# Performance work log

Hardware: AMD Instinct MI355X
Metric: run time of the kernel (lower is better)

## Reference

```python
import jax, jax.numpy as jnp
import numpy as np

BITS = 4
QMAX = (1 << BITS) - 1      # 15
QHALF = 1 << (BITS - 1)     # 8
B, S = 4, 2048
IN, OUT, FP = 4096, 4096, 256
INT = IN - FP


def setup_inputs() -> dict:
    key = jax.random.key(0)
    k0, k1, k2, k3 = jax.random.split(key, 4)
    x = jax.random.normal(k0, (B, S, IN), dtype=jnp.float16)
    # disjoint outlier / int feature index sets (QUIK splits columns by outlier-ness)
    perm = np.random.default_rng(0).permutation(IN)
    fp_indices = jnp.sort(jnp.asarray(perm[:FP], dtype=jnp.int32))
    int_indices = jnp.sort(jnp.asarray(perm[FP:], dtype=jnp.int32))
    # unpacked int4 weight values in [-8, 7] (torch stores these packed 2-per-uint8)
    int_weight = jax.random.randint(k1, (OUT, INT), -QHALF, QHALF, dtype=jnp.int8)
    weights_scales = (jax.random.uniform(k2, (OUT, 1), dtype=jnp.float32) * 0.01 + 1e-3).astype(jnp.float16)
    fp_weight = (jax.random.normal(k3, (OUT, FP), dtype=jnp.float32) * 0.02).astype(jnp.float16)
    bias = jnp.zeros((OUT,), dtype=jnp.float16)
    # reduced_w[j] = w_scale[j] * sum_k int_weight[j, k]  (precomputed zero-point correction)
    reduced_w = (weights_scales.astype(jnp.float32)[:, 0] * jnp.sum(int_weight.astype(jnp.float32), axis=1)).reshape(1, OUT).astype(jnp.float16)
    return {"x": x, "int_weight": int_weight, "fp_weight": fp_weight, "bias": bias,
            "weights_scales": weights_scales, "reduced_w": reduced_w,
            "int_indices": int_indices, "fp_indices": fp_indices}


def reference(x, int_weight, fp_weight, bias, weights_scales, reduced_w, int_indices, fp_indices):
    b, s, in_feat = x.shape
    xf = x.reshape(-1, in_feat)                       # [N, in] tokens
    int_x = xf[:, int_indices].astype(jnp.float32)    # [N, INT]
    fp_x = xf[:, fp_indices].astype(jnp.float32)      # [N, FP] outliers stay fp16-precision
    # asymmetric per-token quantization (quik.asymmetric.quantize)
    mn = jnp.min(int_x, axis=1, keepdims=True)
    mx = jnp.max(int_x, axis=1, keepdims=True)
    scale = jnp.maximum((mx - mn) / QMAX, 1e-8)       # [N,1]
    q = (jnp.clip(jnp.round((int_x - mn) / scale), 0, QMAX) - QHALF).astype(jnp.int8)  # signed int4 in [-8,7]
    zero = scale * QHALF + mn                         # [N,1] shifted zero point
    # int4 GEMM (quik.matmul.int4Matmul), int32 accumulate
    int_res = jnp.einsum('nk,ok->no', q, int_weight, preferred_element_type=jnp.int32)
    # fp outlier branch fused with bias (F.linear)
    fp_res = fp_x @ fp_weight.astype(jnp.float32).T + bias.astype(jnp.float32)[None, :]
    # quik.asymmetric.dequantize: q*scale_x*scale_w + zero_x*reduced_w + fp_result
    out = (int_res.astype(jnp.float32) * scale * weights_scales.astype(jnp.float32)[:, 0][None, :]
           + zero * reduced_w.astype(jnp.float32) + fp_res)
    return out.astype(jnp.float16).reshape(b, s, -1)
```

## Files before the change

### kernel.cpp

```cpp
#include <hip/hip_runtime.h>
#include <hip/hip_bf16.h>
#include <stdint.h>

#define N_TOK 8192
#define IN_F  4096
#define OUT_F 4096
#define FP_F  256
#define INT_F 3840
#define PROW  1920

typedef int    v4i   __attribute__((ext_vector_type(4)));
typedef int    v16i  __attribute__((ext_vector_type(16)));
typedef float  v16f  __attribute__((ext_vector_type(16)));
typedef __bf16 bf16x8 __attribute__((ext_vector_type(8)));

#define WS_QP   0u
#define WS_WP   15728640u
#define WS_FPX  23592960u
#define WS_WFP  27787264u
#define WS_F1   29884416u
#define WS_F2   29917184u
#define WS_F3   29949952u
#define WS_NEED 29982720u


__global__ __launch_bounds__(256) void zero_out_kernel(uint4* __restrict__ o) {
  o[(size_t)blockIdx.x * 256 + threadIdx.x] = uint4{0, 0, 0, 0};
}

__global__ __launch_bounds__(256) void prep_kernel(
    const float* __restrict__ x,
    const int* __restrict__ int_idx, const int* __restrict__ fp_idx,
    const int* __restrict__ int_w, const float* __restrict__ fp_w,
    uint8_t* __restrict__ qp, uint8_t* __restrict__ wp,
    __hip_bfloat16* __restrict__ fpx, __hip_bfloat16* __restrict__ wfp,
    float* __restrict__ f1, float* __restrict__ f2, float* __restrict__ f3) {
  __shared__ uint2 qb[240];
  __shared__ float smn[4], smx[4], ssum[4];
  __shared__ float s_mn, s_inv, s_sc;

  int tid = threadIdx.x;
  int blk = blockIdx.x;

  if (blk >= N_TOK) {
    int pb = blk - N_TOK;
    if (pb < OUT_F * 480 / 256) {
      int t = pb * 256 + tid;
      int r = t / 480, u = t % 480;
      int g = u >> 1, h = u & 1;
      const int* src = int_w + (size_t)r * INT_F + g * 16 + h * 4;
      int4 lo = *(const int4*)src;
      int4 hi = *(const int4*)(src + 8);
      uint32_t o = (uint32_t)((lo.x + 8) & 15) | (uint32_t)((hi.x + 8) & 15) << 4 |
                   (uint32_t)((lo.y + 8) & 15) << 8 | (uint32_t)((hi.y + 8) & 15) << 12 |
                   (uint32_t)((lo.z + 8) & 15) << 16 | (uint32_t)((hi.z + 8) & 15) << 20 |
                   (uint32_t)((lo.w + 8) & 15) << 24 | (uint32_t)((hi.w + 8) & 15) << 28;
      int gs = (g & ~7) | ((g & 7) ^ ((r >> 1) & 7));
      ((uint32_t*)wp)[(size_t)r * 480 + gs * 2 + h] = o;
    } else {
      int t = (pb - OUT_F * 480 / 256) * 256 + tid;
      int i = t * 4;
      int r = i >> 8, c = i & 255;
      float4 v = *(const float4*)(fp_w + i);
      __hip_bfloat16 b[4] = {__float2bfloat16(v.x), __float2bfloat16(v.y),
                             __float2bfloat16(v.z), __float2bfloat16(v.w)};
      int cs = (c & ~0x18) | (((((c) >> 3) & 3) ^ ((r >> 1) & 3)) << 3);
      *(uint2*)(wfp + (size_t)r * 256 + cs) = *(const uint2*)b;
    }
    return;
  }

  int n = blk;
  const float* xr = x + (size_t)n * IN_F;

  float v[15];
  float lmn = 1e30f, lmx = -1e30f;
#pragma unroll
  for (int k = 0; k < 15; k++) {
    v[k] = xr[int_idx[tid + 256 * k]];
    lmn = fminf(lmn, v[k]);
    lmx = fmaxf(lmx, v[k]);
  }
  {
    int sw2 = (n >> 1) & 3;
    int cs = (tid & ~0x18) | ((((tid >> 3) & 3) ^ sw2) << 3);
    fpx[(size_t)n * FP_F + cs] = __float2bfloat16(xr[fp_idx[tid]]);
  }

#pragma unroll
  for (int off = 32; off > 0; off >>= 1) {
    lmn = fminf(lmn, __shfl_xor(lmn, off, 64));
    lmx = fmaxf(lmx, __shfl_xor(lmx, off, 64));
  }
  int wv = tid >> 6, ln = tid & 63;
  if (ln == 0) { smn[wv] = lmn; smx[wv] = lmx; }
  __syncthreads();
  if (tid == 0) {
    float mn = fminf(fminf(smn[0], smn[1]), fminf(smn[2], smn[3]));
    float mx = fmaxf(fmaxf(smx[0], smx[1]), fmaxf(smx[2], smx[3]));
    float sc = fmaxf((mx - mn) / 15.0f, 1e-8f);
    s_mn = mn; s_sc = sc; s_inv = 1.0f / sc;
    f1[n] = sc; f3[n] = mn;
  }
  __syncthreads();
  float mn = s_mn, inv = s_inv;

  uint8_t* qbb = (uint8_t*)qb;
  int swq = (n >> 1) & 7;
  float lsum = 0.0f;
#pragma unroll
  for (int k = 0; k < 15; k++) {
    float c = fminf(fmaxf(rintf((v[k] - mn) * inv), 0.0f), 15.0f);
    lsum += c;
    float ch = __shfl_down(c, 8, 64);
    if ((tid & 15) < 8) {
      int G = (tid >> 4) + 16 * k;
      int pos = ((G & ~7) | ((G & 7) ^ swq)) * 8 + (tid & 7);
      qbb[pos] = (uint8_t)((uint32_t)c | ((uint32_t)ch << 4));
    }
  }
#pragma unroll
  for (int off = 32; off > 0; off >>= 1) lsum += __shfl_xor(lsum, off, 64);
  if (ln == 0) ssum[wv] = lsum;
  __syncthreads();
  if (tid == 0)
    f2[n] = -8.0f * (ssum[0] + ssum[1] + ssum[2] + ssum[3]) * s_sc;
  if (tid < 240)
    *(uint2*)(qp + (size_t)n * PROW + tid * 8) = qb[tid];
}

__device__ inline v4i unpack_nib(uint2 u) {
  v4i r;
  r[0] = (int)(u.x & 0x0F0F0F0Fu);
  r[1] = (int)(u.y & 0x0F0F0F0Fu);
  r[2] = (int)((u.x >> 4) & 0x0F0F0F0Fu);
  r[3] = (int)((u.y >> 4) & 0x0F0F0F0Fu);
  return r;
}

__device__ __forceinline__ void gl16(const void* g, void* l) {
  __builtin_amdgcn_global_load_lds(
      (const __attribute__((address_space(1))) void*)g,
      (__attribute__((address_space(3))) void*)l, 16, 0, 0);
}

__global__ __launch_bounds__(512, 2) void gemm_kernel(
    const uint8_t* __restrict__ qp, const uint8_t* __restrict__ wp,
    const __hip_bfloat16* __restrict__ fpx, const __hip_bfloat16* __restrict__ wfp,
    const float* __restrict__ f1, const float* __restrict__ f2,
    const float* __restrict__ f3,
    const float* __restrict__ wscale, const float* __restrict__ reduced,
    const float* __restrict__ bias, float* __restrict__ out) {
  __shared__ int4 lds4[4096];
  int8_t* lds = (int8_t*)lds4;

  int tid = threadIdx.x;
  int wave = tid >> 6, lane = tid & 63;
  int wm = wave >> 2, wn = wave & 3;
  int blk = blockIdx.x;
  int wg = (blk & 7) * 64 + (blk >> 3);
  int tileM = wg & 31, tileN = wg >> 5;
  int n0 = tileM * 256, o0 = tileN * 256;

  union { v16i i; v16f f; } acc[4][2];
#pragma unroll
  for (int mi = 0; mi < 4; mi++)
#pragma unroll
    for (int ni = 0; ni < 2; ni++)
#pragma unroll
      for (int e = 0; e < 16; e++) acc[mi][ni].i[e] = 0;

  int m = lane & 31, kg = lane >> 5;

  int row0 = tid >> 2, q16b = (tid & 3) * 16;
  int l0 = tid * 16;
  const uint8_t* gA0 = qp + (size_t)(n0 + row0) * PROW + q16b;
  const uint8_t* gA1 = qp + (size_t)(n0 + 128 + row0) * PROW + q16b;
  const uint8_t* gB0 = wp + (size_t)(o0 + row0) * PROW + q16b;
  const uint8_t* gB1 = wp + (size_t)(o0 + 128 + row0) * PROW + q16b;

  gl16(gA0, lds + l0);              gl16(gA1, lds + 8192 + l0);
  gl16(gB0, lds + 16384 + l0);      gl16(gB1, lds + 16384 + 8192 + l0);
  asm volatile("s_waitcnt vmcnt(0)" ::: "memory");
  __builtin_amdgcn_s_barrier();

#pragma unroll 1
  for (int t = 0; t < 30; t++) {
    int ab = (t & 1) << 15;
    int RA = ab, RB = ab + 16384;
    int SA = ab ^ 32768, SB = (ab ^ 32768) + 16384;
    int koff = (t + 1) * 64;
    bool pf = (t < 29);
#pragma unroll
    for (int p = 0; p < 4; p++) {
      int s8 = p * 2 + kg;
      uint2 pa[4], pb[2];
#pragma unroll
      for (int mi = 0; mi < 4; mi++) {
        int row = wm * 128 + mi * 32 + m;
        pa[mi] = *(const uint2*)&lds[RA + row * 64 + ((s8 ^ ((row >> 1) & 7)) * 8)];
      }
#pragma unroll
      for (int ni = 0; ni < 2; ni++) {
        int row = wn * 64 + ni * 32 + m;
        pb[ni] = *(const uint2*)&lds[RB + row * 64 + ((s8 ^ ((row >> 1) & 7)) * 8)];
      }
      if (p == 0 && pf) { gl16(gA0 + koff, lds + SA + l0); gl16(gA1 + koff, lds + SA + 8192 + l0); }
      if (p == 1 && pf) { gl16(gB0 + koff, lds + SB + l0); gl16(gB1 + koff, lds + SB + 8192 + l0); }
      __builtin_amdgcn_s_barrier();
      asm volatile("s_waitcnt lgkmcnt(0)" ::: "memory");
      __builtin_amdgcn_sched_barrier(0);
      __builtin_amdgcn_s_setprio(1);
      v4i a[4], b[2];
#pragma unroll
      for (int mi = 0; mi < 4; mi++) a[mi] = unpack_nib(pa[mi]);
#pragma unroll
      for (int ni = 0; ni < 2; ni++) b[ni] = unpack_nib(pb[ni]);
#pragma unroll
      for (int mi = 0; mi < 4; mi++)
#pragma unroll
        for (int ni = 0; ni < 2; ni++)
          acc[mi][ni].i = __builtin_amdgcn_mfma_i32_32x32x32_i8(
              a[mi], b[ni], acc[mi][ni].i, 0, 0, 0);
      __builtin_amdgcn_s_setprio(0);
      if (p == 3) asm volatile("s_waitcnt vmcnt(0)" ::: "memory");
      __builtin_amdgcn_s_barrier();
    }
  }

  const uint8_t* fxb = (const uint8_t*)fpx;
  const uint8_t* fwb = (const uint8_t*)wfp;
  const uint8_t* gFA0 = fxb + (size_t)(n0 + row0) * 512 + q16b;
  const uint8_t* gFA1 = fxb + (size_t)(n0 + 128 + row0) * 512 + q16b;
  const uint8_t* gFB0 = fwb + (size_t)(o0 + row0) * 512 + q16b;
  const uint8_t* gFB1 = fwb + (size_t)(o0 + 128 + row0) * 512 + q16b;

#define STAGE_BF(SBASE, kr) do {                                     \
    gl16(gFA0 + (kr) * 64, lds + (SBASE) + l0);                      \
    gl16(gFA1 + (kr) * 64, lds + (SBASE) + 8192 + l0);               \
    gl16(gFB0 + (kr) * 64, lds + (SBASE) + 16384 + l0);              \
    gl16(gFB1 + (kr) * 64, lds + (SBASE) + 16384 + 8192 + l0);       \
  } while (0)

  STAGE_BF(0, 0);

  int col = lane & 31, rb4 = (lane >> 5) * 4;
  float cws[2], crw[2], cbs[2];
#pragma unroll
  for (int ni = 0; ni < 2; ni++) {
    int o = o0 + wn * 64 + ni * 32 + col;
    cws[ni] = wscale[o]; crw[ni] = reduced[o]; cbs[ni] = bias[o];
  }
#pragma unroll
  for (int mi = 0; mi < 4; mi++) {
#pragma unroll
    for (int reg = 0; reg < 16; reg++) {
      int row = (reg & 3) + 8 * (reg >> 2) + rb4;
      int n = n0 + wm * 128 + mi * 32 + row;
      float a1 = f1[n], a2 = f2[n], a3 = f3[n];
      float d0 = (float)acc[mi][0].i[reg];
      float d1 = (float)acc[mi][1].i[reg];
      acc[mi][0].f[reg] = (d0 * a1 + a2) * cws[0] + a3 * crw[0] + cbs[0];
      acc[mi][1].f[reg] = (d1 * a1 + a2) * cws[1] + a3 * crw[1] + cbs[1];
    }
  }
  asm volatile("s_waitcnt vmcnt(0)" ::: "memory");
  __builtin_amdgcn_s_barrier();

#pragma unroll 1
  for (int r = 0; r < 8; r++) {
    int ab = (r & 1) << 15;
    int RA = ab, RB = ab + 16384;
    int SA = ab ^ 32768;
    bool pf = (r < 7);
#pragma unroll
    for (int u = 0; u < 2; u++) {
      int s16 = u * 2 + kg;
      bf16x8 a[4], b[2];
#pragma unroll
      for (int mi = 0; mi < 4; mi++) {
        int row = wm * 128 + mi * 32 + m;
        a[mi] = *(const bf16x8*)&lds[RA + row * 64 + ((s16 ^ ((row >> 1) & 3)) * 16)];
      }
#pragma unroll
      for (int ni = 0; ni < 2; ni++) {
        int row = wn * 64 + ni * 32 + m;
        b[ni] = *(const bf16x8*)&lds[RB + row * 64 + ((s16 ^ ((row >> 1) & 3)) * 16)];
      }
      if (u == 0 && pf) STAGE_BF(SA, r + 1);
      __builtin_amdgcn_s_barrier();
      asm volatile("s_waitcnt lgkmcnt(0)" ::: "memory");
      __builtin_amdgcn_sched_barrier(0);
      __builtin_amdgcn_s_setprio(1);
#pragma unroll
      for (int mi = 0; mi < 4; mi++)
#pragma unroll
        for (int ni = 0; ni < 2; ni++)
          acc[mi][ni].f = __builtin_amdgcn_mfma_f32_32x32x16_bf16(
              a[mi], b[ni], acc[mi][ni].f, 0, 0, 0);
      __builtin_amdgcn_s_setprio(0);
      if (u == 1) asm volatile("s_waitcnt vmcnt(0)" ::: "memory");
      __builtin_amdgcn_s_barrier();
    }
  }
#undef STAGE_BF

#pragma unroll
  for (int mi = 0; mi < 4; mi++) {
#pragma unroll
    for (int ni = 0; ni < 2; ni++) {
      int o = o0 + wn * 64 + ni * 32 + col;
#pragma unroll
      for (int reg = 0; reg < 16; reg++) {
        int row = (reg & 3) + 8 * (reg >> 2) + rb4;
        int n = n0 + wm * 128 + mi * 32 + row;
        out[(size_t)n * OUT_F + o] = acc[mi][ni].f[reg];
      }
    }
  }
}

extern "C" void kernel_launch(void* const* d_in, const int* in_sizes, int n_in,
                              void* d_out, int out_size, void* d_ws, size_t ws_size,
                              hipStream_t stream) {
  const float* x     = (const float*)d_in[0];
  const int*   int_w = (const int*)d_in[1];
  const float* fp_w  = (const float*)d_in[2];
  const float* bias  = (const float*)d_in[3];
  const float* wsc   = (const float*)d_in[4];
  const float* red   = (const float*)d_in[5];
  const int*   iidx  = (const int*)d_in[6];
  const int*   fidx  = (const int*)d_in[7];
  float*       out   = (float*)d_out;

  if (ws_size < (size_t)WS_NEED) {
    zero_out_kernel<<<out_size / 1024, 256, 0, stream>>>((uint4*)d_out);
    return;
  }

  uint8_t* ws = (uint8_t*)d_ws;
  uint8_t*        qp  = ws + WS_QP;
  uint8_t*        wpk = ws + WS_WP;
  __hip_bfloat16* fpx = (__hip_bfloat16*)(ws + WS_FPX);
  __hip_bfloat16* wfp = (__hip_bfloat16*)(ws + WS_WFP);
  float*          f1  = (float*)(ws + WS_F1);
  float*          f2  = (float*)(ws + WS_F2);
  float*          f3  = (float*)(ws + WS_F3);

  prep_kernel<<<N_TOK + OUT_F * 480 / 256 + OUT_F * FP_F / 4 / 256, 256, 0, stream>>>(
      x, iidx, fidx, int_w, fp_w, qp, wpk, fpx, wfp, f1, f2, f3);
  gemm_kernel<<<(N_TOK / 256) * (OUT_F / 256), 512, 0, stream>>>(
      qp, wpk, fpx, wfp, f1, f2, f3, wsc, red, bias, out);
}
```

Measured before the change: 420.1 us.

## Store int4 operands as unpacked bytes and triple-buffer GEMM LDS stages

Activations and weights are now stored one value per byte instead of two nibbles per byte. The GEMM therefore feeds i8 MFMA directly without nibble unpacking ALU work, at the cost of twice the global and LDS traffic and more K iterations. The GEMM moves from double to triple buffering with a deeper prefetch, using vmcnt(4) waits. The prep kernel now handles one token per wavefront with shuffle-only reductions, which removes shared-memory barriers.

```diff
diff --git a/kernel.cpp b/kernel.cpp
--- a/kernel.cpp
+++ b/kernel.cpp
@@ -7,7 +7,6 @@
 #define OUT_F 4096
 #define FP_F  256
 #define INT_F 3840
-#define PROW  1920
 
 typedef int    v4i   __attribute__((ext_vector_type(4)));
 typedef int    v16i  __attribute__((ext_vector_type(16)));
@@ -15,50 +14,45 @@
 typedef __bf16 bf16x8 __attribute__((ext_vector_type(8)));
 
 #define WS_QP   0u
-#define WS_WP   15728640u
-#define WS_FPX  23592960u
-#define WS_WFP  27787264u
-#define WS_F1   29884416u
-#define WS_F2   29917184u
-#define WS_F3   29949952u
-#define WS_NEED 29982720u
+#define WS_WP   31457280u
+#define WS_FPX  47185920u
+#define WS_WFP  51380224u
+#define WS_F1   53477376u
+#define WS_F2   53510144u
+#define WS_F3   53542912u
+#define WS_NEED 53575680u
 
 
 __global__ __launch_bounds__(256) void zero_out_kernel(uint4* __restrict__ o) {
   o[(size_t)blockIdx.x * 256 + threadIdx.x] = uint4{0, 0, 0, 0};
 }
 
-__global__ __launch_bounds__(256) void prep_kernel(
+__global__ __launch_bounds__(256, 4) void prep_kernel(
     const float* __restrict__ x,
     const int* __restrict__ int_idx, const int* __restrict__ fp_idx,
     const int* __restrict__ int_w, const float* __restrict__ fp_w,
     uint8_t* __restrict__ qp, uint8_t* __restrict__ wp,
     __hip_bfloat16* __restrict__ fpx, __hip_bfloat16* __restrict__ wfp,
     float* __restrict__ f1, float* __restrict__ f2, float* __restrict__ f3) {
-  __shared__ uint2 qb[240];
-  __shared__ float smn[4], smx[4], ssum[4];
-  __shared__ float s_mn, s_inv, s_sc;
-
   int tid = threadIdx.x;
   int blk = blockIdx.x;
 
-  if (blk >= N_TOK) {
-    int pb = blk - N_TOK;
-    if (pb < OUT_F * 480 / 256) {
+  if (blk >= 2048) {
+    int pb = blk - 2048;
+    if (pb < 15360) {
       int t = pb * 256 + tid;
-      int r = t / 480, u = t % 480;
-      int g = u >> 1, h = u & 1;
-      const int* src = int_w + (size_t)r * INT_F + g * 16 + h * 4;
-      int4 lo = *(const int4*)src;
-      int4 hi = *(const int4*)(src + 8);
-      uint32_t o = (uint32_t)((lo.x + 8) & 15) | (uint32_t)((hi.x + 8) & 15) << 4 |
-                   (uint32_t)((lo.y + 8) & 15) << 8 | (uint32_t)((hi.y + 8) & 15) << 12 |
-                   (uint32_t)((lo.z + 8) & 15) << 16 | (uint32_t)((hi.z + 8) & 15) << 20 |
-                   (uint32_t)((lo.w + 8) & 15) << 24 | (uint32_t)((hi.w + 8) & 15) << 28;
-      int gs = (g & ~7) | ((g & 7) ^ ((r >> 1) & 7));
-      ((uint32_t*)wp)[(size_t)r * 480 + gs * 2 + h] = o;
+      int r = t / 960, u = t % 960;
+      const int* src = int_w + (size_t)r * INT_F + u * 4;
+      int4 w4 = *(const int4*)src;
+      uint32_t pk = (uint32_t)((w4.x + 8) & 15) |
+                    (uint32_t)((w4.y + 8) & 15) << 8 |
+                    (uint32_t)((w4.z + 8) & 15) << 16 |
+                    (uint32_t)((w4.w + 8) & 15) << 24;
+      int g = u >> 2;
+      int gp = (g & ~3) | ((g & 3) ^ ((r >> 1) & 3));
+      ((uint32_t*)wp)[(size_t)r * 960 + gp * 4 + (u & 3)] = pk;
     } else {
-      int t = (pb - OUT_F * 480 / 256) * 256 + tid;
+      int t = (pb - 15360) * 256 + tid;
       int i = t * 4;
       int r = i >> 8, c = i & 255;
       float4 v = *(const float4*)(fp_w + i);
@@ -70,21 +64,31 @@
     return;
   }
 
-  int n = blk;
+  int wave = tid >> 6, l = tid & 63;
+  int n = blk * 4 + wave;
   const float* xr = x + (size_t)n * IN_F;
 
-  float v[15];
+  float v[60];
   float lmn = 1e30f, lmx = -1e30f;
 #pragma unroll
   for (int k = 0; k < 15; k++) {
-    v[k] = xr[int_idx[tid + 256 * k]];
-    lmn = fminf(lmn, v[k]);
-    lmx = fmaxf(lmx, v[k]);
+    int4 id = *(const int4*)&int_idx[4 * l + 256 * k];
+    v[4 * k + 0] = xr[id.x]; v[4 * k + 1] = xr[id.y];
+    v[4 * k + 2] = xr[id.z]; v[4 * k + 3] = xr[id.w];
+#pragma unroll
+    for (int j = 0; j < 4; j++) {
+      lmn = fminf(lmn, v[4 * k + j]);
+      lmx = fmaxf(lmx, v[4 * k + j]);
+    }
   }
   {
     int sw2 = (n >> 1) & 3;
-    int cs = (tid & ~0x18) | ((((tid >> 3) & 3) ^ sw2) << 3);
-    fpx[(size_t)n * FP_F + cs] = __float2bfloat16(xr[fp_idx[tid]]);
+#pragma unroll
+    for (int j = 0; j < 4; j++) {
+      int c = l + 64 * j;
+      int cs = (c & ~0x18) | ((((c >> 3) & 3) ^ sw2) << 3);
+      fpx[(size_t)n * FP_F + cs] = __float2bfloat16(xr[fp_idx[c]]);
+    }
   }
 
 #pragma unroll
@@ -92,50 +96,30 @@
     lmn = fminf(lmn, __shfl_xor(lmn, off, 64));
     lmx = fmaxf(lmx, __shfl_xor(lmx, off, 64));
   }
-  int wv = tid >> 6, ln = tid & 63;
-  if (ln == 0) { smn[wv] = lmn; smx[wv] = lmx; }
-  __syncthreads();
-  if (tid == 0) {
-    float mn = fminf(fminf(smn[0], smn[1]), fminf(smn[2], smn[3]));
-    float mx = fmaxf(fmaxf(smx[0], smx[1]), fmaxf(smx[2], smx[3]));
-    float sc = fmaxf((mx - mn) / 15.0f, 1e-8f);
-    s_mn = mn; s_sc = sc; s_inv = 1.0f / sc;
-    f1[n] = sc; f3[n] = mn;
-  }
-  __syncthreads();
-  float mn = s_mn, inv = s_inv;
-
-  uint8_t* qbb = (uint8_t*)qb;
-  int swq = (n >> 1) & 7;
+  float mn = lmn;
+  float sc = fmaxf((lmx - mn) / 15.0f, 1e-8f);
+  float inv = 1.0f / sc;
+  if (l == 0) { f1[n] = sc; f3[n] = mn; }
+
+  int sw4 = (n >> 1) & 3;
+  uint32_t* qrow = (uint32_t*)(qp + (size_t)n * INT_F);
   float lsum = 0.0f;
 #pragma unroll
   for (int k = 0; k < 15; k++) {
-    float c = fminf(fmaxf(rintf((v[k] - mn) * inv), 0.0f), 15.0f);
-    lsum += c;
-    float ch = __shfl_down(c, 8, 64);
-    if ((tid & 15) < 8) {
-      int G = (tid >> 4) + 16 * k;
-      int pos = ((G & ~7) | ((G & 7) ^ swq)) * 8 + (tid & 7);
-      qbb[pos] = (uint8_t)((uint32_t)c | ((uint32_t)ch << 4));
-    }
+    uint32_t pk = 0;
+#pragma unroll
+    for (int j = 0; j < 4; j++) {
+      float c = fminf(fmaxf(rintf((v[4 * k + j] - mn) * inv), 0.0f), 15.0f);
+      lsum += c;
+      pk |= (uint32_t)c << (8 * j);
+    }
+    int g = (l >> 2) + 16 * k;
+    int gp = (g & ~3) | ((g & 3) ^ sw4);
+    qrow[gp * 4 + (l & 3)] = pk;
   }
 #pragma unroll
   for (int off = 32; off > 0; off >>= 1) lsum += __shfl_xor(lsum, off, 64);
-  if (ln == 0) ssum[wv] = lsum;
-  __syncthreads();
-  if (tid == 0)
-    f2[n] = -8.0f * (ssum[0] + ssum[1] + ssum[2] + ssum[3]) * s_sc;
-  if (tid < 240)
-    *(uint2*)(qp + (size_t)n * PROW + tid * 8) = qb[tid];
-}
-
-__device__ inline v4i unpack_nib(uint2 u) {
-  v4i r;
-  r[0] = (int)(u.x & 0x0F0F0F0Fu);
-  r[1] = (int)(u.y & 0x0F0F0F0Fu);
-  r[2] = (int)((u.x >> 4) & 0x0F0F0F0Fu);
-  r[3] = (int)((u.y >> 4) & 0x0F0F0F0Fu);
-  return r;
+  if (l == 0) f2[n] = -8.0f * lsum * sc;
 }
 
 __device__ __forceinline__ void gl16(const void* g, void* l) {
@@ -151,7 +135,7 @@
     const float* __restrict__ f3,
     const float* __restrict__ wscale, const float* __restrict__ reduced,
     const float* __restrict__ bias, float* __restrict__ out) {
-  __shared__ int4 lds4[4096];
+  __shared__ int4 lds4[6144];
   int8_t* lds = (int8_t*)lds4;
 
   int tid = threadIdx.x;
@@ -174,48 +158,49 @@
 
   int row0 = tid >> 2, q16b = (tid & 3) * 16;
   int l0 = tid * 16;
-  const uint8_t* gA0 = qp + (size_t)(n0 + row0) * PROW + q16b;
-  const uint8_t* gA1 = qp + (size_t)(n0 + 128 + row0) * PROW + q16b;
-  const uint8_t* gB0 = wp + (size_t)(o0 + row0) * PROW + q16b;
-  const uint8_t* gB1 = wp + (size_t)(o0 + 128 + row0) * PROW + q16b;
-
-  gl16(gA0, lds + l0);              gl16(gA1, lds + 8192 + l0);
-  gl16(gB0, lds + 16384 + l0);      gl16(gB1, lds + 16384 + 8192 + l0);
-  asm volatile("s_waitcnt vmcnt(0)" ::: "memory");
+  const uint8_t* gA0 = qp + (size_t)(n0 + row0) * INT_F + q16b;
+  const uint8_t* gA1 = qp + (size_t)(n0 + 128 + row0) * INT_F + q16b;
+  const uint8_t* gB0 = wp + (size_t)(o0 + row0) * INT_F + q16b;
+  const uint8_t* gB1 = wp + (size_t)(o0 + 128 + row0) * INT_F + q16b;
+
+#define STAGE_A(base, kt) do {                                   \
+    gl16(gA0 + (kt) * 64, lds + (base) + l0);                    \
+    gl16(gA1 + (kt) * 64, lds + (base) + 8192 + l0);             \
+  } while (0)
+#define STAGE_B(base, kt) do {                                   \
+    gl16(gB0 + (kt) * 64, lds + (base) + 16384 + l0);            \
+    gl16(gB1 + (kt) * 64, lds + (base) + 24576 + l0);            \
+  } while (0)
+
+  STAGE_A(0, 0); STAGE_B(0, 0);
+  STAGE_A(32768, 1); STAGE_B(32768, 1);
+  asm volatile("s_waitcnt vmcnt(4)" ::: "memory");
   __builtin_amdgcn_s_barrier();
 
 #pragma unroll 1
-  for (int t = 0; t < 30; t++) {
-    int ab = (t & 1) << 15;
-    int RA = ab, RB = ab + 16384;
-    int SA = ab ^ 32768, SB = (ab ^ 32768) + 16384;
-    int koff = (t + 1) * 64;
-    bool pf = (t < 29);
-#pragma unroll
-    for (int p = 0; p < 4; p++) {
-      int s8 = p * 2 + kg;
-      uint2 pa[4], pb[2];
+  for (int t = 0; t < 60; t++) {
+    int rb = (t % 3) * 32768;
+    int sb = ((t + 2) % 3) * 32768;
+    bool st = (t + 2 < 60);
+#pragma unroll
+    for (int ks = 0; ks < 2; ks++) {
+      int s = ks * 2 + kg;
+      v4i a[4], b[2];
 #pragma unroll
       for (int mi = 0; mi < 4; mi++) {
         int row = wm * 128 + mi * 32 + m;
-        pa[mi] = *(const uint2*)&lds[RA + row * 64 + ((s8 ^ ((row >> 1) & 7)) * 8)];
+        a[mi] = *(const v4i*)&lds[rb + row * 64 + ((s ^ ((row >> 1) & 3)) * 16)];
       }
 #pragma unroll
       for (int ni = 0; ni < 2; ni++) {
         int row = wn * 64 + ni * 32 + m;
-        pb[ni] = *(const uint2*)&lds[RB + row * 64 + ((s8 ^ ((row >> 1) & 7)) * 8)];
-      }
-      if (p == 0 && pf) { gl16(gA0 + koff, lds + SA + l0); gl16(gA1 + koff, lds + SA + 8192 + l0); }
-      if (p == 1 && pf) { gl16(gB0 + koff, lds + SB + l0); gl16(gB1 + koff, lds + SB + 8192 + l0); }
+        b[ni] = *(const v4i*)&lds[rb + 16384 + row * 64 + ((s ^ ((row >> 1) & 3)) * 16)];
+      }
+      if (st) { if (ks == 0) STAGE_A(sb, t + 2); else STAGE_B(sb, t + 2); }
       __builtin_amdgcn_s_barrier();
       asm volatile("s_waitcnt lgkmcnt(0)" ::: "memory");
       __builtin_amdgcn_sched_barrier(0);
       __builtin_amdgcn_s_setprio(1);
-      v4i a[4], b[2];
-#pragma unroll
-      for (int mi = 0; mi < 4; mi++) a[mi] = unpack_nib(pa[mi]);
-#pragma unroll
-      for (int ni = 0; ni < 2; ni++) b[ni] = unpack_nib(pb[ni]);
 #pragma unroll
       for (int mi = 0; mi < 4; mi++)
 #pragma unroll
@@ -223,7 +208,10 @@
           acc[mi][ni].i = __builtin_amdgcn_mfma_i32_32x32x32_i8(
               a[mi], b[ni], acc[mi][ni].i, 0, 0, 0);
       __builtin_amdgcn_s_setprio(0);
-      if (p == 3) asm volatile("s_waitcnt vmcnt(0)" ::: "memory");
+      if (ks == 1) {
+        if (t < 58) asm volatile("s_waitcnt vmcnt(4)" ::: "memory");
+        else        asm volatile("s_waitcnt vmcnt(0)" ::: "memory");
+      }
       __builtin_amdgcn_s_barrier();
     }
   }
@@ -235,14 +223,16 @@
   const uint8_t* gFB0 = fwb + (size_t)(o0 + row0) * 512 + q16b;
   const uint8_t* gFB1 = fwb + (size_t)(o0 + 128 + row0) * 512 + q16b;
 
-#define STAGE_BF(SBASE, kr) do {                                     \
-    gl16(gFA0 + (kr) * 64, lds + (SBASE) + l0);                      \
-    gl16(gFA1 + (kr) * 64, lds + (SBASE) + 8192 + l0);               \
-    gl16(gFB0 + (kr) * 64, lds + (SBASE) + 16384 + l0);              \
-    gl16(gFB1 + (kr) * 64, lds + (SBASE) + 16384 + 8192 + l0);       \
+#define STAGE_FA(base, kr) do {                                  \
+    gl16(gFA0 + (kr) * 64, lds + (base) + l0);                   \
+    gl16(gFA1 + (kr) * 64, lds + (base) + 8192 + l0);            \
   } while (0)
-
-  STAGE_BF(0, 0);
+#define STAGE_FB(base, kr) do {                                  \
+    gl16(gFB0 + (kr) * 64, lds + (base) + 16384 + l0);           \
+    gl16(gFB1 + (kr) * 64, lds + (base) + 24576 + l0);           \
+  } while (0)
+
+  STAGE_FA(0, 0); STAGE_FB(0, 0);
 
   int col = lane & 31, rb4 = (lane >> 5) * 4;
   float cws[2], crw[2], cbs[2];
@@ -264,30 +254,29 @@
       acc[mi][1].f[reg] = (d1 * a1 + a2) * cws[1] + a3 * crw[1] + cbs[1];
     }
   }
-  asm volatile("s_waitcnt vmcnt(0)" ::: "memory");
+  STAGE_FA(32768, 1); STAGE_FB(32768, 1);
   __builtin_amdgcn_s_barrier();
 
 #pragma unroll 1
   for (int r = 0; r < 8; r++) {
-    int ab = (r & 1) << 15;
-    int RA = ab, RB = ab + 16384;
-    int SA = ab ^ 32768;
-    bool pf = (r < 7);
+    int rb = (r % 3) * 32768;
+    int sb = ((r + 2) % 3) * 32768;
+    bool st = (r + 2 < 8);
 #pragma unroll
     for (int u = 0; u < 2; u++) {
-      int s16 = u * 2 + kg;
+      int s = u * 2 + kg;
       bf16x8 a[4], b[2];
 #pragma unroll
       for (int mi = 0; mi < 4; mi++) {
         int row = wm * 128 + mi * 32 + m;
-        a[mi] = *(const bf16x8*)&lds[RA + row * 64 + ((s16 ^ ((row >> 1) & 3)) * 16)];
+        a[mi] = *(const bf16x8*)&lds[rb + row * 64 + ((s ^ ((row >> 1) & 3)) * 16)];
       }
 #pragma unroll
       for (int ni = 0; ni < 2; ni++) {
         int row = wn * 64 + ni * 32 + m;
-        b[ni] = *(const bf16x8*)&lds[RB + row * 64 + ((s16 ^ ((row >> 1) & 3)) * 16)];
-      }
-      if (u == 0 && pf) STAGE_BF(SA, r + 1);
+        b[ni] = *(const bf16x8*)&lds[rb + 16384 + row * 64 + ((s ^ ((row >> 1) & 3)) * 16)];
+      }
+      if (st) { if (u == 0) STAGE_FA(sb, r + 2); else STAGE_FB(sb, r + 2); }
       __builtin_amdgcn_s_barrier();
       asm volatile("s_waitcnt lgkmcnt(0)" ::: "memory");
       __builtin_amdgcn_sched_barrier(0);
@@ -299,11 +288,17 @@
           acc[mi][ni].f = __builtin_amdgcn_mfma_f32_32x32x16_bf16(
               a[mi], b[ni], acc[mi][ni].f, 0, 0, 0);
       __builtin_amdgcn_s_setprio(0);
-      if (u == 1) asm volatile("s_waitcnt vmcnt(0)" ::: "memory");
+      if (u == 1) {
+        if (r < 6) asm volatile("s_waitcnt vmcnt(4)" ::: "memory");
+        else       asm volatile("s_waitcnt vmcnt(0)" ::: "memory");
+      }
       __builtin_amdgcn_s_barrier();
     }
   }
-#undef STAGE_BF
+#undef STAGE_A
+#undef STAGE_B
+#undef STAGE_FA
+#undef STAGE_FB
 
 #pragma unroll
   for (int mi = 0; mi < 4; mi++) {
@@ -347,7 +342,7 @@
   float*          f2  = (float*)(ws + WS_F2);
   float*          f3  = (float*)(ws + WS_F3);
 
-  prep_kernel<<<N_TOK + OUT_F * 480 / 256 + OUT_F * FP_F / 4 / 256, 256, 0, stream>>>(
+  prep_kernel<<<2048 + 15360 + 1024, 256, 0, stream>>>(
       x, iidx, fidx, int_w, fp_w, qp, wpk, fpx, wfp, f1, f2, f3);
   gemm_kernel<<<(N_TOK / 256) * (OUT_F / 256), 512, 0, stream>>>(
       qp, wpk, fpx, wfp, f1, f2, f3, wsc, red, bias, out);
```

After: 441.3 us. 5.0% more time.
